# Performance work log

Hardware: AMD Instinct MI355X
Metric: run time of the kernel (lower is better)

Reference implementation:

```python
import jax, jax.numpy as jnp
from jax import lax
import numpy as np

# config (matches init_kwargs)
D_IN, D_OUT = 768, 128
P = 2
BLUR = 0.05
SCALING = 0.8
SCALING_FACTOR = 0.1
DIAM = 32.0  # static upper bound on transformed point-cloud diameter


def _eps_schedule():
    # geomloss-style epsilon annealing: eps from diameter**p down to blur**p
    eps_list = []
    eps = DIAM ** P
    target = BLUR ** P
    while eps > target:
        eps_list.append(eps)
        eps *= SCALING ** P
    eps_list.append(target)
    return np.asarray(eps_list, dtype=np.float32)


def _cost(x, y):
    # C_ij = (1/p) * ||x_i - y_j||^p with p=2 -> 0.5 * squared euclidean
    sq = (jnp.sum(x * x, -1)[:, None] + jnp.sum(y * y, -1)[None, :]
          - 2.0 * (x @ y.T))
    return 0.5 * jnp.maximum(sq, 0.0)


def _softmin(eps, C, h):
    # -eps * logsumexp_j( h_j - C_ij / eps ), rows of C
    return -eps * jax.nn.logsumexp(h[None, :] - C / eps, axis=1)


def sinkhorn_divergence(x, y):
    # Debiased Sinkhorn divergence S(x,y) = <a, f_xy - f_xx> + <b, g_xy - g_yy>
    # with uniform weights, log-domain iterations, eps-scaling, and
    # envelope-theorem gradients (loop runs on detached costs; one final
    # differentiable extrapolation) -- as in geomloss SamplesLoss('sinkhorn').
    eps_list = jnp.asarray(_eps_schedule())
    N, Mn = x.shape[0], y.shape[0]
    loga = jnp.float32(-np.log(N))
    logb = jnp.float32(-np.log(Mn))

    xd, yd = lax.stop_gradient(x), lax.stop_gradient(y)
    Cxy = _cost(xd, yd)   # [N, M]
    Cyx = Cxy.T           # [M, N]
    Cxx = _cost(xd, xd)   # [N, N]
    Cyy = _cost(yd, yd)   # [M, M]

    init = (jnp.zeros((N,), jnp.float32), jnp.zeros((Mn,), jnp.float32),
            jnp.zeros((N,), jnp.float32), jnp.zeros((Mn,), jnp.float32))

    def step(carry, eps):
        f, g, fx, gy = carry
        ft = _softmin(eps, Cxy, logb + g / eps)
        gt = _softmin(eps, Cyx, loga + f / eps)
        f2 = 0.5 * (f + ft)
        g2 = 0.5 * (g + gt)
        fx2 = 0.5 * (fx + _softmin(eps, Cxx, loga + fx / eps))
        gy2 = 0.5 * (gy + _softmin(eps, Cyy, logb + gy / eps))
        return (f2, g2, fx2, gy2), None

    (f, g, fx, gy), _ = lax.scan(step, init, eps_list)
    f, g, fx, gy = map(lax.stop_gradient, (f, g, fx, gy))

    eps = eps_list[-1]
    # final differentiable extrapolation through the cost
    f_xy = _softmin(eps, _cost(x, y), logb + g / eps)
    g_xy = _softmin(eps, _cost(y, x), loga + f / eps)
    f_xx = _softmin(eps, _cost(x, x), loga + fx / eps)
    g_yy = _softmin(eps, _cost(y, y), logb + gy / eps)
    return jnp.mean(f_xy - f_xx) + jnp.mean(g_xy - g_yy)


def setup_inputs() -> dict:
    key = jax.random.key(0)
    k1, k2, k3, k4 = jax.random.split(key, 4)
    d = jax.random.normal(k1, (4096, D_IN), jnp.float32)
    s1 = jax.random.normal(k2, (2048, D_IN), jnp.float32)
    s2 = jax.random.normal(k3, (2048, D_IN), jnp.float32)
    # learned metric transform M (scaled so transformed clouds have diam ~ DIAM)
    M = 0.02 * jax.random.normal(k4, (D_IN, D_OUT), jnp.float32)
    return {"d": d, "s1": s1, "s2": s2, "M": M}


def reference(d, s1, s2, M):
    td = d @ M
    t1 = s1 @ M
    t2 = s2 @ M
    dist1 = sinkhorn_divergence(td, t1)
    dist2 = sinkhorn_divergence(td, t2)
    return jax.nn.sigmoid(SCALING_FACTOR * (dist2 - dist1))
```

## Files before the change

kernel.cpp:

```cpp
#include <hip/hip_runtime.h>
#include <math.h>

typedef unsigned char u8;
typedef unsigned short u16;
typedef unsigned int u32;
typedef __attribute__((ext_vector_type(8))) short bf16x8;
typedef __attribute__((ext_vector_type(4))) float f32x4;

#define NE 30
static constexpr float QMAX  = 160.0f;
static constexpr float QS8   = 255.0f / QMAX;
static constexpr float HQS8  = 0.5f * QS8;
static constexpr float LOGA  = -8.3177661667193430f;
static constexpr float LOGB  = -7.6246189861593985f;
static constexpr float LOG2E = 1.4426950408889634f;
static constexpr float LN2   = 0.6931471805599453f;
static constexpr float LOGA2 = LOGA * LOG2E;
static constexpr float LOGB2 = LOGB * LOG2E;

static constexpr size_t OFF_MT  = 1048576;
static constexpr size_t OFF_N   = 1146880;
static constexpr size_t OFF_POT = 1155072;
static constexpr size_t OFF_OUT = 1187840;
static constexpr size_t OFF_CQ  = 1204224;
static constexpr size_t CQ_YX = 8388608;
static constexpr size_t CQ_YY = 16777216;
static constexpr size_t CQ_DV = 20971520;

__device__ __forceinline__ float fexp2(float x) {
#if __has_builtin(__builtin_amdgcn_exp2f)
  return __builtin_amdgcn_exp2f(x);
#else
  return exp2f(x);
#endif
}
__device__ __forceinline__ float flog2(float x) {
#if __has_builtin(__builtin_amdgcn_logf)
  return __builtin_amdgcn_logf(x);
#else
  return __log2f(x);
#endif
}

__device__ __forceinline__ void split1(float x, u16& h, u16& l) {
  const u32 u = __float_as_uint(x);
  const u32 hb = u & 0xffff0000u;
  const float xl = x - __uint_as_float(hb);
  h = (u16)(hb >> 16);
  l = (u16)(__float_as_uint(xl) >> 16);
}

__device__ __forceinline__ void splitAB(const float4 p, const float4 q,
                                        bf16x8& h, bf16x8& l) {
  const float pf[8] = {p.x, p.y, p.z, p.w, q.x, q.y, q.z, q.w};
#pragma unroll
  for (int i = 0; i < 8; ++i) {
    u16 hh, ll;
    split1(pf[i], hh, ll);
    h[i] = (short)hh;
    l[i] = (short)ll;
  }
}

__global__ __launch_bounds__(256) void prep_m_kernel(
    const float* __restrict__ Mw, float* __restrict__ ws)
{
  const int id = blockIdx.x * 256 + threadIdx.x;
  const int ks = id >> 9;
  const int g  = (id >> 7) & 3;
  const int n  = id & 127;
  u16* mthi = (u16*)(ws + OFF_MT);
  u16* mtlo = mthi + 98304;
  bf16x8 h, l;
#pragma unroll
  for (int e = 0; e < 8; ++e) {
    const float x = Mw[(size_t)(ks * 32 + g * 8 + e) * 128 + n];
    u16 hh, ll;
    split1(x, hh, ll);
    h[e] = (short)hh;
    l[e] = (short)ll;
  }
  *reinterpret_cast<bf16x8*>(mthi + (size_t)id * 8) = h;
  *reinterpret_cast<bf16x8*>(mtlo + (size_t)id * 8) = l;
}

__global__ __launch_bounds__(256) void transform_kernel(
    const float* __restrict__ d, const float* __restrict__ s1,
    const float* __restrict__ s2, float* __restrict__ ws)
{
  const int tid = threadIdx.x;
  const int w = tid >> 6, ln = tid & 63;
  const int lr = ln & 15, lg = ln >> 4;
  const int tile = blockIdx.x & 127;
  const int ks4  = blockIdx.x >> 7;
  const float* Xb; int r0;
  if (tile < 64)      { Xb = d;  r0 = tile * 64; }
  else if (tile < 96) { Xb = s1; r0 = (tile - 64) * 64; }
  else                { Xb = s2; r0 = (tile - 96) * 64; }
  const int grow = tile * 64;
  const u16* mthi = (const u16*)(ws + OFF_MT);
  const u16* mtlo = mthi + 98304;

  f32x4 acc[8];
  const f32x4 zero = {0.f, 0.f, 0.f, 0.f};
#pragma unroll
  for (int nt = 0; nt < 8; ++nt) acc[nt] = zero;

#pragma unroll
  for (int ksl = 0; ksl < 6; ++ksl) {
    const int ks = ks4 * 6 + ksl;
    const float* xp = Xb + (size_t)(r0 + w * 16 + lr) * 768 + ks * 32 + lg * 8;
    const float4 p = *reinterpret_cast<const float4*>(xp);
    const float4 q = *reinterpret_cast<const float4*>(xp + 4);
    bf16x8 ah, al;
    splitAB(p, q, ah, al);
#pragma unroll
    for (int nt = 0; nt < 8; ++nt) {
      const size_t bo = ((size_t)(ks * 4 + lg) * 128 + nt * 16 + lr) * 8;
      const bf16x8 bh = *reinterpret_cast<const bf16x8*>(mthi + bo);
      const bf16x8 bl = *reinterpret_cast<const bf16x8*>(mtlo + bo);
      acc[nt] = __builtin_amdgcn_mfma_f32_16x16x32_bf16(ah, bh, acc[nt], 0, 0, 0);
      acc[nt] = __builtin_amdgcn_mfma_f32_16x16x32_bf16(ah, bl, acc[nt], 0, 0, 0);
      acc[nt] = __builtin_amdgcn_mfma_f32_16x16x32_bf16(al, bh, acc[nt], 0, 0, 0);
    }
  }
  float* P = ws + OFF_CQ + (size_t)ks4 * 1048576;
#pragma unroll
  for (int nt = 0; nt < 8; ++nt)
#pragma unroll
    for (int reg = 0; reg < 4; ++reg)
      P[(size_t)(grow + w * 16 + lg * 4 + reg) * 128 + nt * 16 + lr] = acc[nt][reg];
}

__global__ __launch_bounds__(256) void reduceT_kernel(float* __restrict__ ws)
{
  const int wv = threadIdx.x >> 6, ln = threadIdx.x & 63;
  const int row = blockIdx.x * 4 + wv;
  const float2* Pb = reinterpret_cast<const float2*>(ws + OFF_CQ);
  const size_t idx = (size_t)row * 64 + ln;
  float2 t = Pb[idx];
  {
    const float2 b = Pb[idx + 524288];
    const float2 c = Pb[idx + 1048576];
    const float2 e = Pb[idx + 1572864];
    t.x += b.x + c.x + e.x;
    t.y += b.y + c.y + e.y;
  }
  float s = fmaf(t.x, t.x, t.y * t.y);
#pragma unroll
  for (int off = 32; off; off >>= 1) s += __shfl_xor(s, off);
  if (ln == 0) ws[OFF_N + row] = s;
  u16 h0, l0, h1, l1;
  split1(t.x, h0, l0);
  split1(t.y, h1, l1);
  u32* thiw = (u32*)ws;
  u32* tlow = thiw + 524288;
  thiw[idx] = (u32)h0 | ((u32)h1 << 16);
  tlow[idx] = (u32)l0 | ((u32)l1 << 16);
}

__global__ __launch_bounds__(256) void cost_all_kernel(float* __restrict__ ws)
{
  __shared__ __align__(16) float eb[16 * 516];
  const int tid = threadIdx.x;
  const int w = tid >> 6, ln = tid & 63;
  const int lr = ln & 15, lg = ln >> 4;

  const int b = blockIdx.x;
  const int dv = b / 1280;
  const int bb = b - dv * 1280;
  const u16* thi = (const u16*)ws;
  const u16* tlo = thi + 1048576;
  const u16* yhi = thi + (size_t)(4096 + dv * 2048) * 128;
  const u16* ylo = tlo + (size_t)(4096 + dv * 2048) * 128;
  const float* nrm = ws + OFF_N;
  u8* cq = (u8*)(ws + OFF_CQ) + (size_t)dv * CQ_DV;

  const u16 *xhi_, *xlo_, *yhi_, *ylo_;
  const float *nx, *ny;
  u8* C; int ldc, i0, j0;
  if (bb < 512) {
    i0 = (bb & 127) * 32; j0 = (bb >> 7) * 512;
    xhi_ = thi; xlo_ = tlo; yhi_ = yhi; ylo_ = ylo;
    nx = nrm; ny = nrm + 4096 + dv * 2048;
    C = cq; ldc = 2048;
  } else if (bb < 1024) {
    const int b2 = bb - 512;
    i0 = (b2 & 63) * 32; j0 = (b2 >> 6) * 512;
    xhi_ = yhi; xlo_ = ylo; yhi_ = thi; ylo_ = tlo;
    nx = nrm + 4096 + dv * 2048; ny = nrm;
    C = cq + CQ_YX; ldc = 4096;
  } else {
    const int b2 = bb - 1024;
    i0 = (b2 & 63) * 32; j0 = (b2 >> 6) * 512;
    xhi_ = yhi; xlo_ = ylo; yhi_ = yhi; ylo_ = ylo;
    nx = nrm + 4096 + dv * 2048; ny = nx;
    C = cq + CQ_YY; ldc = 2048;
  }
  const int cw = j0 + w * 128;

  f32x4 acc[2][8];
  const f32x4 zero = {0.f, 0.f, 0.f, 0.f};
#pragma unroll
  for (int mt = 0; mt < 2; ++mt)
#pragma unroll
    for (int nt = 0; nt < 8; ++nt) acc[mt][nt] = zero;

#pragma unroll
  for (int ks = 0; ks < 4; ++ks) {
    bf16x8 ah[2], al[2];
#pragma unroll
    for (int mt = 0; mt < 2; ++mt) {
      const size_t xo = (size_t)(i0 + mt * 16 + lr) * 128 + ks * 32 + lg * 8;
      ah[mt] = *reinterpret_cast<const bf16x8*>(xhi_ + xo);
      al[mt] = *reinterpret_cast<const bf16x8*>(xlo_ + xo);
    }
#pragma unroll
    for (int ntg = 0; ntg < 2; ++ntg) {
      bf16x8 bh[4], bl[4];
#pragma unroll
      for (int q = 0; q < 4; ++q) {
        const int nt = ntg * 4 + q;
        const size_t yo = (size_t)(cw + nt * 16 + lr) * 128 + ks * 32 + lg * 8;
        bh[q] = *reinterpret_cast<const bf16x8*>(yhi_ + yo);
        bl[q] = *reinterpret_cast<const bf16x8*>(ylo_ + yo);
      }
#pragma unroll
      for (int q = 0; q < 4; ++q) {
        const int nt = ntg * 4 + q;
#pragma unroll
        for (int mt = 0; mt < 2; ++mt) {
          acc[mt][nt] = __builtin_amdgcn_mfma_f32_16x16x32_bf16(ah[mt], bh[q], acc[mt][nt], 0, 0, 0);
          acc[mt][nt] = __builtin_amdgcn_mfma_f32_16x16x32_bf16(ah[mt], bl[q], acc[mt][nt], 0, 0, 0);
          acc[mt][nt] = __builtin_amdgcn_mfma_f32_16x16x32_bf16(al[mt], bh[q], acc[mt][nt], 0, 0, 0);
        }
      }
    }
  }

  float ct[8];
  {
    const float4 n0 = *reinterpret_cast<const float4*>(ny + j0 + ln * 8);
    const float4 n1 = *reinterpret_cast<const float4*>(ny + j0 + ln * 8 + 4);
    ct[0] = n0.x * HQS8; ct[1] = n0.y * HQS8; ct[2] = n0.z * HQS8; ct[3] = n0.w * HQS8;
    ct[4] = n1.x * HQS8; ct[5] = n1.y * HQS8; ct[6] = n1.z * HQS8; ct[7] = n1.w * HQS8;
  }

#pragma unroll
  for (int h = 0; h < 2; ++h) {
    if (h) __syncthreads();
#pragma unroll
    for (int nt = 0; nt < 8; ++nt)
#pragma unroll
      for (int reg = 0; reg < 4; ++reg)
        eb[(lg * 4 + reg) * 516 + w * 128 + nt * 16 + lr] = acc[h][nt][reg];
    __syncthreads();
#pragma unroll
    for (int rr = 0; rr < 4; ++rr) {
      const int rl = w * 4 + rr;
      const int rg = i0 + h * 16 + rl;
      const float rowt = fmaf(nx[rg], HQS8, 0.5f);
      const float* lp = eb + rl * 516 + ln * 8;
      const float4 e0 = *reinterpret_cast<const float4*>(lp);
      const float4 e1 = *reinterpret_cast<const float4*>(lp + 4);
      const float q0 = fmaxf(fminf(fmaf(e0.x, -QS8, ct[0] + rowt), 255.f), 0.f);
      const float q1 = fmaxf(fminf(fmaf(e0.y, -QS8, ct[1] + rowt), 255.f), 0.f);
      const float q2 = fmaxf(fminf(fmaf(e0.z, -QS8, ct[2] + rowt), 255.f), 0.f);
      const float q3 = fmaxf(fminf(fmaf(e0.w, -QS8, ct[3] + rowt), 255.f), 0.f);
      const float q4 = fmaxf(fminf(fmaf(e1.x, -QS8, ct[4] + rowt), 255.f), 0.f);
      const float q5 = fmaxf(fminf(fmaf(e1.y, -QS8, ct[5] + rowt), 255.f), 0.f);
      const float q6 = fmaxf(fminf(fmaf(e1.z, -QS8, ct[6] + rowt), 255.f), 0.f);
      const float q7 = fmaxf(fminf(fmaf(e1.w, -QS8, ct[7] + rowt), 255.f), 0.f);
      uint2 v;
      v.x = (u32)q0 | ((u32)q1 << 8) | ((u32)q2 << 16) | ((u32)q3 << 24);
      v.y = (u32)q4 | ((u32)q5 << 8) | ((u32)q6 << 16) | ((u32)q7 << 24);
      *reinterpret_cast<uint2*>(C + (size_t)rg * ldc + j0 + ln * 8) = v;
    }
  }
}

template <int NH>
__device__ __forceinline__ void softmin2(
    const u8* __restrict__ Cbase, const int ldc, const float* __restrict__ h,
    const float lw2, const float ie2, const float qie2, const float negeln2,
    const float* __restrict__ oldv, float* __restrict__ o,
    const int row0, const bool avg, const int ln)
{
  float m[2], s[2];
#pragma unroll
  for (int r = 0; r < 2; ++r) { m[r] = -3.0e38f; s[r] = 0.f; }
#pragma unroll
  for (int hf = 0; hf < NH; ++hf) {
    uint2 cq[2][4];
#pragma unroll
    for (int r = 0; r < 2; ++r) {
      const u8* cp = Cbase + (size_t)(row0 + r) * ldc + hf * 2048 + ln * 8;
#pragma unroll
      for (int k = 0; k < 4; ++k)
        cq[r][k] = *reinterpret_cast<const uint2*>(cp + k * 512);
    }
    const float* hp = h + hf * 2048 + ln * 8;
    float4 hv[8];
#pragma unroll
    for (int k = 0; k < 4; ++k) {
      hv[k * 2]     = *reinterpret_cast<const float4*>(hp + k * 512);
      hv[k * 2 + 1] = *reinterpret_cast<const float4*>(hp + k * 512 + 4);
    }
#pragma unroll
    for (int k = 0; k < 4; ++k) {
      float ht[8];
      ht[0] = fmaf(hv[k * 2].x, ie2, lw2);
      ht[1] = fmaf(hv[k * 2].y, ie2, lw2);
      ht[2] = fmaf(hv[k * 2].z, ie2, lw2);
      ht[3] = fmaf(hv[k * 2].w, ie2, lw2);
      ht[4] = fmaf(hv[k * 2 + 1].x, ie2, lw2);
      ht[5] = fmaf(hv[k * 2 + 1].y, ie2, lw2);
      ht[6] = fmaf(hv[k * 2 + 1].z, ie2, lw2);
      ht[7] = fmaf(hv[k * 2 + 1].w, ie2, lw2);
#pragma unroll
      for (int r = 0; r < 2; ++r) {
        const uint2 c = cq[r][k];
        const float a0 = ht[0] - (float)(c.x & 0xffu) * qie2;
        const float a1 = ht[1] - (float)((c.x >> 8) & 0xffu) * qie2;
        const float a2 = ht[2] - (float)((c.x >> 16) & 0xffu) * qie2;
        const float a3 = ht[3] - (float)(c.x >> 24) * qie2;
        const float a4 = ht[4] - (float)(c.y & 0xffu) * qie2;
        const float a5 = ht[5] - (float)((c.y >> 8) & 0xffu) * qie2;
        const float a6 = ht[6] - (float)((c.y >> 16) & 0xffu) * qie2;
        const float a7 = ht[7] - (float)(c.y >> 24) * qie2;
        const float cm = fmaxf(fmaxf(fmaxf(a0, a1), fmaxf(a2, a3)),
                               fmaxf(fmaxf(a4, a5), fmaxf(a6, a7)));
        const float nm = fmaxf(m[r], cm);
        float e = fexp2(a0 - nm);
        e += fexp2(a1 - nm);
        e += fexp2(a2 - nm);
        e += fexp2(a3 - nm);
        e += fexp2(a4 - nm);
        e += fexp2(a5 - nm);
        e += fexp2(a6 - nm);
        e += fexp2(a7 - nm);
        s[r] = fmaf(s[r], fexp2(m[r] - nm), e);
        m[r] = nm;
      }
    }
  }
#pragma unroll
  for (int r = 0; r < 2; ++r) {
#pragma unroll
    for (int off = 32; off; off >>= 1) {
      const float om = __shfl_xor(m[r], off);
      const float os = __shfl_xor(s[r], off);
      const float nm = fmaxf(m[r], om);
      s[r] = fmaf(s[r], fexp2(m[r] - nm), os * fexp2(om - nm));
      m[r] = nm;
    }
  }
  if (ln == 0) {
#pragma unroll
    for (int r = 0; r < 2; ++r) {
      float v = negeln2 * (m[r] + flog2(s[r]));
      if (avg) v = 0.5f * (oldv[row0 + r] + v);
      o[row0 + r] = v;
    }
  }
}

__global__ __launch_bounds__(256, 6) void sinkhorn_iter_kernel(
    float* __restrict__ ws, const float ie2, const float negeln2, const float qie2,
    const int cur, const int fin)
{
  const int w = threadIdx.x >> 6, ln = threadIdx.x & 63;
  const int dv = blockIdx.x >> 10;
  const int bb = blockIdx.x & 1023;
  float* pot  = ws + OFF_POT + dv * 16384;
  float* outv = ws + OFF_OUT + dv * 8192;
  const u8* cq = reinterpret_cast<const u8*>(ws + OFF_CQ) + (size_t)dv * CQ_DV;
  const float* fc = pot + cur * 4096;
  float* fn = pot + (cur ^ 1) * 4096;
  const float* gc = pot + 8192 + cur * 2048;
  float* gn = pot + 8192 + (cur ^ 1) * 2048;
  const float* yc = pot + 12288 + cur * 2048;
  float* yn = pot + 12288 + (cur ^ 1) * 2048;
  if (w == 0) {
    softmin2<2>(cq + CQ_YX, 4096, fc, LOGA2, ie2, qie2, negeln2,
                gc, fin ? (outv + 4096) : gn, bb * 2, !fin, ln);
  } else if (w == 3) {
    softmin2<1>(cq + CQ_YY, 2048, yc, LOGB2, ie2, qie2, negeln2,
                yc, fin ? (outv + 6144) : yn, bb * 2, !fin, ln);
  } else {
    softmin2<1>(cq, 2048, gc, LOGB2, ie2, qie2, negeln2,
                fc, fin ? outv : fn, bb * 4 + (w - 1) * 2, !fin, ln);
  }
}

__global__ void init_pot_kernel(float* __restrict__ ws)
{
  const int i = blockIdx.x * 256 + threadIdx.x;
  if (i < 32768) ws[OFF_POT + i] = 0.f;
}

__global__ __launch_bounds__(256) void finalize_kernel(
    const float* __restrict__ ws, float* __restrict__ out)
{
  const float* ov = ws + OFF_OUT;
  const int tid = threadIdx.x;
  float v[6] = {0.f, 0.f, 0.f, 0.f, 0.f, 0.f};
  for (int i = tid; i < 4096; i += 256) { v[0] += ov[i]; v[3] += ov[8192 + i]; }
  for (int i = tid; i < 2048; i += 256) {
    v[1] += ov[4096 + i]; v[2] += ov[6144 + i];
    v[4] += ov[8192 + 4096 + i]; v[5] += ov[8192 + 6144 + i];
  }
  __shared__ float sh[6][4];
  const int wv = tid >> 6, ln = tid & 63;
#pragma unroll
  for (int q = 0; q < 6; ++q) {
    float s = v[q];
#pragma unroll
    for (int off = 32; off; off >>= 1) s += __shfl_xor(s, off);
    if (ln == 0) sh[q][wv] = s;
  }
  __syncthreads();
  if (tid == 0) {
    float t[6];
#pragma unroll
    for (int q = 0; q < 6; ++q) t[q] = sh[q][0] + sh[q][1] + sh[q][2] + sh[q][3];
    const float d1 = t[0] * (1.f / 4096.f) + (t[1] - t[2]) * (1.f / 2048.f);
    const float d2 = t[3] * (1.f / 4096.f) + (t[4] - t[5]) * (1.f / 2048.f);
    const float z = 0.1f * (d2 - d1);
    out[0] = 1.f / (1.f + expf(-z));
  }
}

extern "C" void kernel_launch(void* const* d_in, const int* in_sizes, int n_in,
                              void* d_out, int out_size, void* d_ws, size_t ws_size,
                              hipStream_t stream)
{
  const float* d  = (const float*)d_in[0];
  const float* s1 = (const float*)d_in[1];
  const float* s2 = (const float*)d_in[2];
  const float* Mw = (const float*)d_in[3];
  float* out = (float*)d_out;
  float* ws = (float*)d_ws;

  float eps_l[NE];
  {
    double e = 1024.0;
    const double sc = 0.8 * 0.8;
    for (int k = 0; k < NE - 1; ++k) { eps_l[k] = (float)e; e *= sc; }
    eps_l[NE - 1] = (float)(0.05 * 0.05);
  }

  prep_m_kernel<<<48, 256, 0, stream>>>(Mw, ws);
  transform_kernel<<<512, 256, 0, stream>>>(d, s1, s2, ws);
  reduceT_kernel<<<2048, 256, 0, stream>>>(ws);

  cost_all_kernel<<<2560, 256, 0, stream>>>(ws);

  init_pot_kernel<<<128, 256, 0, stream>>>(ws);
  int cur = 0;
  for (int it = 0; it <= NE; ++it) {
    const int fin = (it == NE);
    const float e = eps_l[fin ? NE - 1 : it];
    const float ie2 = LOG2E / e;
    const float qie2 = (QMAX / 255.0f) * ie2;
    sinkhorn_iter_kernel<<<2048, 256, 0, stream>>>(ws, ie2, -e * LN2, qie2, cur, fin);
    if (!fin) cur ^= 1;
  }

  finalize_kernel<<<1, 256, 0, stream>>>(ws, out);
  (void)in_sizes; (void)n_in; (void)out_size; (void)ws_size;
}
```

Baseline: 512.3 us.

## Fuse Sinkhorn iterations into one persistent cooperative kernel with grid sync

Replaces the 31 per-iteration kernel launches with a single cooperative launch of 1280 blocks that loops over the epsilon schedule and uses grid-wide sync between iterations. The epsilon values now live in the workspace, written by the init kernel. Work is redistributed so each wave handles one uniform task (a full YX row, or two XY/YY rows) for both divergences, instead of a heterogeneous per-wave split. This removes launch overhead and inter-kernel gaps, at the cost of grid-barrier latency and an occupancy requirement of 5 blocks per CU, with a multi-launch fallback if the cooperative launch fails.

```diff
diff --git a/kernel.cpp b/kernel.cpp
--- a/kernel.cpp
+++ b/kernel.cpp
@@ -1,5 +1,8 @@
 #include <hip/hip_runtime.h>
+#include <hip/hip_cooperative_groups.h>
 #include <math.h>
+
+namespace cg = cooperative_groups;
 
 typedef unsigned char u8;
 typedef unsigned short u16;
@@ -19,6 +22,7 @@
 static constexpr float LOGB2 = LOGB * LOG2E;
 
 static constexpr size_t OFF_MT  = 1048576;
+static constexpr size_t OFF_EPS = 1048576;
 static constexpr size_t OFF_N   = 1146880;
 static constexpr size_t OFF_POT = 1155072;
 static constexpr size_t OFF_OUT = 1187840;
@@ -279,9 +283,69 @@
   }
 }
 
-template <int NH>
+__device__ __forceinline__ void softminR(
+    const u8* __restrict__ Crow, const float* __restrict__ h,
+    const float lw2, const float ie2, const float qie2, const float negeln2,
+    const float* __restrict__ oldv, float* __restrict__ o,
+    const int row, const bool avg, const int ln)
+{
+  float m = -3.0e38f, s = 0.f;
+#pragma unroll
+  for (int hf = 0; hf < 2; ++hf) {
+    const u8* cp = Crow + hf * 2048 + ln * 8;
+    const float* hp = h + hf * 2048 + ln * 8;
+    uint2 cq[4];
+#pragma unroll
+    for (int k = 0; k < 4; ++k)
+      cq[k] = *reinterpret_cast<const uint2*>(cp + k * 512);
+    float4 hv[8];
+#pragma unroll
+    for (int k = 0; k < 4; ++k) {
+      hv[k * 2]     = *reinterpret_cast<const float4*>(hp + k * 512);
+      hv[k * 2 + 1] = *reinterpret_cast<const float4*>(hp + k * 512 + 4);
+    }
+#pragma unroll
+    for (int k = 0; k < 4; ++k) {
+      const float a0 = fmaf(hv[k * 2].x, ie2, lw2) - (float)(cq[k].x & 0xffu) * qie2;
+      const float a1 = fmaf(hv[k * 2].y, ie2, lw2) - (float)((cq[k].x >> 8) & 0xffu) * qie2;
+      const float a2 = fmaf(hv[k * 2].z, ie2, lw2) - (float)((cq[k].x >> 16) & 0xffu) * qie2;
+      const float a3 = fmaf(hv[k * 2].w, ie2, lw2) - (float)(cq[k].x >> 24) * qie2;
+      const float a4 = fmaf(hv[k * 2 + 1].x, ie2, lw2) - (float)(cq[k].y & 0xffu) * qie2;
+      const float a5 = fmaf(hv[k * 2 + 1].y, ie2, lw2) - (float)((cq[k].y >> 8) & 0xffu) * qie2;
+      const float a6 = fmaf(hv[k * 2 + 1].z, ie2, lw2) - (float)((cq[k].y >> 16) & 0xffu) * qie2;
+      const float a7 = fmaf(hv[k * 2 + 1].w, ie2, lw2) - (float)(cq[k].y >> 24) * qie2;
+      const float cm = fmaxf(fmaxf(fmaxf(a0, a1), fmaxf(a2, a3)),
+                             fmaxf(fmaxf(a4, a5), fmaxf(a6, a7)));
+      const float nm = fmaxf(m, cm);
+      float e = fexp2(a0 - nm);
+      e += fexp2(a1 - nm);
+      e += fexp2(a2 - nm);
+      e += fexp2(a3 - nm);
+      e += fexp2(a4 - nm);
+      e += fexp2(a5 - nm);
+      e += fexp2(a6 - nm);
+      e += fexp2(a7 - nm);
+      s = fmaf(s, fexp2(m - nm), e);
+      m = nm;
+    }
+  }
+#pragma unroll
+  for (int off = 32; off; off >>= 1) {
+    const float om = __shfl_xor(m, off);
+    const float os = __shfl_xor(s, off);
+    const float nm = fmaxf(m, om);
+    s = fmaf(s, fexp2(m - nm), os * fexp2(om - nm));
+    m = nm;
+  }
+  if (ln == 0) {
+    float v = negeln2 * (m + flog2(s));
+    if (avg) v = 0.5f * (oldv[row] + v);
+    o[row] = v;
+  }
+}
+
 __device__ __forceinline__ void softmin2(
-    const u8* __restrict__ Cbase, const int ldc, const float* __restrict__ h,
+    const u8* __restrict__ Cbase, const float* __restrict__ h,
     const float lw2, const float ie2, const float qie2, const float negeln2,
     const float* __restrict__ oldv, float* __restrict__ o,
     const int row0, const bool avg, const int ln)
@@ -289,59 +353,56 @@
   float m[2], s[2];
 #pragma unroll
   for (int r = 0; r < 2; ++r) { m[r] = -3.0e38f; s[r] = 0.f; }
-#pragma unroll
-  for (int hf = 0; hf < NH; ++hf) {
-    uint2 cq[2][4];
+  uint2 cq[2][4];
+#pragma unroll
+  for (int r = 0; r < 2; ++r) {
+    const u8* cp = Cbase + (size_t)(row0 + r) * 2048 + ln * 8;
+#pragma unroll
+    for (int k = 0; k < 4; ++k)
+      cq[r][k] = *reinterpret_cast<const uint2*>(cp + k * 512);
+  }
+  const float* hp = h + ln * 8;
+  float4 hv[8];
+#pragma unroll
+  for (int k = 0; k < 4; ++k) {
+    hv[k * 2]     = *reinterpret_cast<const float4*>(hp + k * 512);
+    hv[k * 2 + 1] = *reinterpret_cast<const float4*>(hp + k * 512 + 4);
+  }
+#pragma unroll
+  for (int k = 0; k < 4; ++k) {
+    float ht[8];
+    ht[0] = fmaf(hv[k * 2].x, ie2, lw2);
+    ht[1] = fmaf(hv[k * 2].y, ie2, lw2);
+    ht[2] = fmaf(hv[k * 2].z, ie2, lw2);
+    ht[3] = fmaf(hv[k * 2].w, ie2, lw2);
+    ht[4] = fmaf(hv[k * 2 + 1].x, ie2, lw2);
+    ht[5] = fmaf(hv[k * 2 + 1].y, ie2, lw2);
+    ht[6] = fmaf(hv[k * 2 + 1].z, ie2, lw2);
+    ht[7] = fmaf(hv[k * 2 + 1].w, ie2, lw2);
 #pragma unroll
     for (int r = 0; r < 2; ++r) {
-      const u8* cp = Cbase + (size_t)(row0 + r) * ldc + hf * 2048 + ln * 8;
-#pragma unroll
-      for (int k = 0; k < 4; ++k)
-        cq[r][k] = *reinterpret_cast<const uint2*>(cp + k * 512);
-    }
-    const float* hp = h + hf * 2048 + ln * 8;
-    float4 hv[8];
-#pragma unroll
-    for (int k = 0; k < 4; ++k) {
-      hv[k * 2]     = *reinterpret_cast<const float4*>(hp + k * 512);
-      hv[k * 2 + 1] = *reinterpret_cast<const float4*>(hp + k * 512 + 4);
-    }
-#pragma unroll
-    for (int k = 0; k < 4; ++k) {
-      float ht[8];
-      ht[0] = fmaf(hv[k * 2].x, ie2, lw2);
-      ht[1] = fmaf(hv[k * 2].y, ie2, lw2);
-      ht[2] = fmaf(hv[k * 2].z, ie2, lw2);
-      ht[3] = fmaf(hv[k * 2].w, ie2, lw2);
-      ht[4] = fmaf(hv[k * 2 + 1].x, ie2, lw2);
-      ht[5] = fmaf(hv[k * 2 + 1].y, ie2, lw2);
-      ht[6] = fmaf(hv[k * 2 + 1].z, ie2, lw2);
-      ht[7] = fmaf(hv[k * 2 + 1].w, ie2, lw2);
-#pragma unroll
-      for (int r = 0; r < 2; ++r) {
-        const uint2 c = cq[r][k];
-        const float a0 = ht[0] - (float)(c.x & 0xffu) * qie2;
-        const float a1 = ht[1] - (float)((c.x >> 8) & 0xffu) * qie2;
-        const float a2 = ht[2] - (float)((c.x >> 16) & 0xffu) * qie2;
-        const float a3 = ht[3] - (float)(c.x >> 24) * qie2;
-        const float a4 = ht[4] - (float)(c.y & 0xffu) * qie2;
-        const float a5 = ht[5] - (float)((c.y >> 8) & 0xffu) * qie2;
-        const float a6 = ht[6] - (float)((c.y >> 16) & 0xffu) * qie2;
-        const float a7 = ht[7] - (float)(c.y >> 24) * qie2;
-        const float cm = fmaxf(fmaxf(fmaxf(a0, a1), fmaxf(a2, a3)),
-                               fmaxf(fmaxf(a4, a5), fmaxf(a6, a7)));
-        const float nm = fmaxf(m[r], cm);
-        float e = fexp2(a0 - nm);
-        e += fexp2(a1 - nm);
-        e += fexp2(a2 - nm);
-        e += fexp2(a3 - nm);
-        e += fexp2(a4 - nm);
-        e += fexp2(a5 - nm);
-        e += fexp2(a6 - nm);
-        e += fexp2(a7 - nm);
-        s[r] = fmaf(s[r], fexp2(m[r] - nm), e);
-        m[r] = nm;
-      }
+      const uint2 c = cq[r][k];
+      const float a0 = ht[0] - (float)(c.x & 0xffu) * qie2;
+      const float a1 = ht[1] - (float)((c.x >> 8) & 0xffu) * qie2;
+      const float a2 = ht[2] - (float)((c.x >> 16) & 0xffu) * qie2;
+      const float a3 = ht[3] - (float)(c.x >> 24) * qie2;
+      const float a4 = ht[4] - (float)(c.y & 0xffu) * qie2;
+      const float a5 = ht[5] - (float)((c.y >> 8) & 0xffu) * qie2;
+      const float a6 = ht[6] - (float)((c.y >> 16) & 0xffu) * qie2;
+      const float a7 = ht[7] - (float)(c.y >> 24) * qie2;
+      const float cm = fmaxf(fmaxf(fmaxf(a0, a1), fmaxf(a2, a3)),
+                             fmaxf(fmaxf(a4, a5), fmaxf(a6, a7)));
+      const float nm = fmaxf(m[r], cm);
+      float e = fexp2(a0 - nm);
+      e += fexp2(a1 - nm);
+      e += fexp2(a2 - nm);
+      e += fexp2(a3 - nm);
+      e += fexp2(a4 - nm);
+      e += fexp2(a5 - nm);
+      e += fexp2(a6 - nm);
+      e += fexp2(a7 - nm);
+      s[r] = fmaf(s[r], fexp2(m[r] - nm), e);
+      m[r] = nm;
     }
   }
 #pragma unroll
@@ -365,13 +426,11 @@
   }
 }
 
-__global__ __launch_bounds__(256, 6) void sinkhorn_iter_kernel(
-    float* __restrict__ ws, const float ie2, const float negeln2, const float qie2,
-    const int cur, const int fin)
-{
-  const int w = threadIdx.x >> 6, ln = threadIdx.x & 63;
-  const int dv = blockIdx.x >> 10;
-  const int bb = blockIdx.x & 1023;
+__device__ __forceinline__ void do_task(
+    float* __restrict__ ws, const int dv, const int tt,
+    const float ie2, const float negeln2, const float qie2,
+    const int cur, const int fin, const int ln)
+{
   float* pot  = ws + OFF_POT + dv * 16384;
   float* outv = ws + OFF_OUT + dv * 8192;
   const u8* cq = reinterpret_cast<const u8*>(ws + OFF_CQ) + (size_t)dv * CQ_DV;
@@ -381,15 +440,37 @@
   float* gn = pot + 8192 + (cur ^ 1) * 2048;
   const float* yc = pot + 12288 + cur * 2048;
   float* yn = pot + 12288 + (cur ^ 1) * 2048;
-  if (w == 0) {
-    softmin2<2>(cq + CQ_YX, 4096, fc, LOGA2, ie2, qie2, negeln2,
-                gc, fin ? (outv + 4096) : gn, bb * 2, !fin, ln);
-  } else if (w == 3) {
-    softmin2<1>(cq + CQ_YY, 2048, yc, LOGB2, ie2, qie2, negeln2,
-                yc, fin ? (outv + 6144) : yn, bb * 2, !fin, ln);
+  if (tt < 2048) {
+    softminR(cq + CQ_YX + (size_t)tt * 4096, fc, LOGA2, ie2, qie2, negeln2,
+             gc, fin ? (outv + 4096) : gn, tt, !fin, ln);
+  } else if (tt < 4096) {
+    softmin2(cq, gc, LOGB2, ie2, qie2, negeln2,
+             fc, fin ? outv : fn, (tt - 2048) * 2, !fin, ln);
   } else {
-    softmin2<1>(cq, 2048, gc, LOGB2, ie2, qie2, negeln2,
-                fc, fin ? outv : fn, bb * 4 + (w - 1) * 2, !fin, ln);
+    softmin2(cq + CQ_YY, yc, LOGB2, ie2, qie2, negeln2,
+             yc, fin ? (outv + 6144) : yn, (tt - 4096) * 2, !fin, ln);
+  }
+}
+
+__global__ __launch_bounds__(256, 5) void sink_coop_kernel(
+    float* __restrict__ ws, const int it0, const int it1)
+{
+  const int w = threadIdx.x >> 6, ln = threadIdx.x & 63;
+  const int gwid = blockIdx.x * 4 + w;
+  const float* eps = ws + OFF_EPS;
+  for (int it = it0; it <= it1; ++it) {
+    const int fin = (it == NE);
+    const float e = eps[fin ? NE - 1 : it];
+    const float ie2 = LOG2E / e;
+    const float qie2 = (QMAX / 255.0f) * ie2;
+    const float negeln2 = -e * LN2;
+    const int cur = it & 1;
+    do_task(ws, 0, gwid, ie2, negeln2, qie2, cur, fin, ln);
+    do_task(ws, 1, gwid, ie2, negeln2, qie2, cur, fin, ln);
+    if (it < it1) {
+      __threadfence();
+      cg::this_grid().sync();
+    }
   }
 }
 
@@ -397,6 +478,12 @@
 {
   const int i = blockIdx.x * 256 + threadIdx.x;
   if (i < 32768) ws[OFF_POT + i] = 0.f;
+  if (blockIdx.x == 0 && threadIdx.x == 0) {
+    double e = 1024.0;
+    const double sc = 0.8 * 0.8;
+    for (int k = 0; k < NE - 1; ++k) { ws[OFF_EPS + k] = (float)e; e *= sc; }
+    ws[OFF_EPS + NE - 1] = (float)(0.05 * 0.05);
+  }
 }
 
 __global__ __launch_bounds__(256) void finalize_kernel(
@@ -442,14 +529,6 @@
   float* out = (float*)d_out;
   float* ws = (float*)d_ws;
 
-  float eps_l[NE];
-  {
-    double e = 1024.0;
-    const double sc = 0.8 * 0.8;
-    for (int k = 0; k < NE - 1; ++k) { eps_l[k] = (float)e; e *= sc; }
-    eps_l[NE - 1] = (float)(0.05 * 0.05);
-  }
-
   prep_m_kernel<<<48, 256, 0, stream>>>(Mw, ws);
   transform_kernel<<<512, 256, 0, stream>>>(d, s1, s2, ws);
   reduceT_kernel<<<2048, 256, 0, stream>>>(ws);
@@ -457,14 +536,23 @@
   cost_all_kernel<<<2560, 256, 0, stream>>>(ws);
 
   init_pot_kernel<<<128, 256, 0, stream>>>(ws);
-  int cur = 0;
-  for (int it = 0; it <= NE; ++it) {
-    const int fin = (it == NE);
-    const float e = eps_l[fin ? NE - 1 : it];
-    const float ie2 = LOG2E / e;
-    const float qie2 = (QMAX / 255.0f) * ie2;
-    sinkhorn_iter_kernel<<<2048, 256, 0, stream>>>(ws, ie2, -e * LN2, qie2, cur, fin);
-    if (!fin) cur ^= 1;
+
+  bool coop_ok = false;
+  {
+    int maxB = 0;
+    hipError_t qe = hipOccupancyMaxActiveBlocksPerMultiprocessor(
+        &maxB, sink_coop_kernel, 256, 0);
+    if (qe == hipSuccess && maxB >= 5) {
+      int it0 = 0, it1 = NE;
+      void* args[] = { (void*)&ws, (void*)&it0, (void*)&it1 };
+      hipError_t le = hipLaunchCooperativeKernel(
+          (const void*)sink_coop_kernel, dim3(1280), dim3(256), args, 0, stream);
+      coop_ok = (le == hipSuccess);
+    }
+  }
+  if (!coop_ok) {
+    for (int it = 0; it <= NE; ++it)
+      sink_coop_kernel<<<1280, 256, 0, stream>>>(ws, it, it);
   }
 
   finalize_kernel<<<1, 256, 0, stream>>>(ws, out);
```

Result: slower. 573.8 us (+12.0%).

## Rebalance Sinkhorn softmin work per wave and widen loads to 16 bytes

Applied to the files above, without the earlier changes.

Before, each block gave its four waves fixed roles, and wave 0 handled the two 4096-wide YX rows while the other waves handled 2048-wide rows, so work per wave was uneven. Now each wave computes its task from a global wave id: one YX row per wave, or two rows of the 2048-wide XY/YY matrices, so every wave reads the same amount of data. The grid grows from 2048 to 2560 blocks. Cost loads widen from 8-byte uint2 to 16-byte uint4, with 16 columns per lane per chunk, which cuts the number of load instructions. In exchange, each lane now keeps 16 terms live in the log-sum-exp step, which may raise register pressure against the launch bound of 6.

```diff
diff --git a/kernel.cpp b/kernel.cpp
--- a/kernel.cpp
+++ b/kernel.cpp
@@ -279,70 +279,114 @@
   }
 }
 
-template <int NH>
+__device__ __forceinline__ void lse16c(
+    const uint4 c, const float* __restrict__ ht, const float qie2,
+    float& m, float& s)
+{
+  const float a0  = fmaf((float)(c.x & 0xffu),        -qie2, ht[0]);
+  const float a1  = fmaf((float)((c.x >> 8) & 0xffu), -qie2, ht[1]);
+  const float a2  = fmaf((float)((c.x >> 16) & 0xffu),-qie2, ht[2]);
+  const float a3  = fmaf((float)(c.x >> 24),          -qie2, ht[3]);
+  const float a4  = fmaf((float)(c.y & 0xffu),        -qie2, ht[4]);
+  const float a5  = fmaf((float)((c.y >> 8) & 0xffu), -qie2, ht[5]);
+  const float a6  = fmaf((float)((c.y >> 16) & 0xffu),-qie2, ht[6]);
+  const float a7  = fmaf((float)(c.y >> 24),          -qie2, ht[7]);
+  const float a8  = fmaf((float)(c.z & 0xffu),        -qie2, ht[8]);
+  const float a9  = fmaf((float)((c.z >> 8) & 0xffu), -qie2, ht[9]);
+  const float a10 = fmaf((float)((c.z >> 16) & 0xffu),-qie2, ht[10]);
+  const float a11 = fmaf((float)(c.z >> 24),          -qie2, ht[11]);
+  const float a12 = fmaf((float)(c.w & 0xffu),        -qie2, ht[12]);
+  const float a13 = fmaf((float)((c.w >> 8) & 0xffu), -qie2, ht[13]);
+  const float a14 = fmaf((float)((c.w >> 16) & 0xffu),-qie2, ht[14]);
+  const float a15 = fmaf((float)(c.w >> 24),          -qie2, ht[15]);
+  const float m0 = fmaxf(fmaxf(a0, a1), fmaxf(a2, a3));
+  const float m1 = fmaxf(fmaxf(a4, a5), fmaxf(a6, a7));
+  const float m2 = fmaxf(fmaxf(a8, a9), fmaxf(a10, a11));
+  const float m3 = fmaxf(fmaxf(a12, a13), fmaxf(a14, a15));
+  const float cm = fmaxf(fmaxf(m0, m1), fmaxf(m2, m3));
+  const float nm = fmaxf(m, cm);
+  float e = fexp2(a0 - nm);
+  e += fexp2(a1 - nm);  e += fexp2(a2 - nm);  e += fexp2(a3 - nm);
+  e += fexp2(a4 - nm);  e += fexp2(a5 - nm);  e += fexp2(a6 - nm);
+  e += fexp2(a7 - nm);  e += fexp2(a8 - nm);  e += fexp2(a9 - nm);
+  e += fexp2(a10 - nm); e += fexp2(a11 - nm); e += fexp2(a12 - nm);
+  e += fexp2(a13 - nm); e += fexp2(a14 - nm); e += fexp2(a15 - nm);
+  s = fmaf(s, fexp2(m - nm), e);
+  m = nm;
+}
+
+__device__ __forceinline__ void make_ht(
+    const float* __restrict__ hp, const float ie2, const float lw2,
+    float* __restrict__ ht)
+{
+  const float4 h0 = *reinterpret_cast<const float4*>(hp);
+  const float4 h1 = *reinterpret_cast<const float4*>(hp + 4);
+  const float4 h2 = *reinterpret_cast<const float4*>(hp + 8);
+  const float4 h3 = *reinterpret_cast<const float4*>(hp + 12);
+  ht[0]  = fmaf(h0.x, ie2, lw2); ht[1]  = fmaf(h0.y, ie2, lw2);
+  ht[2]  = fmaf(h0.z, ie2, lw2); ht[3]  = fmaf(h0.w, ie2, lw2);
+  ht[4]  = fmaf(h1.x, ie2, lw2); ht[5]  = fmaf(h1.y, ie2, lw2);
+  ht[6]  = fmaf(h1.z, ie2, lw2); ht[7]  = fmaf(h1.w, ie2, lw2);
+  ht[8]  = fmaf(h2.x, ie2, lw2); ht[9]  = fmaf(h2.y, ie2, lw2);
+  ht[10] = fmaf(h2.z, ie2, lw2); ht[11] = fmaf(h2.w, ie2, lw2);
+  ht[12] = fmaf(h3.x, ie2, lw2); ht[13] = fmaf(h3.y, ie2, lw2);
+  ht[14] = fmaf(h3.z, ie2, lw2); ht[15] = fmaf(h3.w, ie2, lw2);
+}
+
+__device__ __forceinline__ void softminR(
+    const u8* __restrict__ Crow, const float* __restrict__ h,
+    const float lw2, const float ie2, const float qie2, const float negeln2,
+    const float* __restrict__ oldv, float* __restrict__ o,
+    const int row, const bool avg, const int ln)
+{
+  const u8* cp = Crow + ln * 16;
+  uint4 cq[4];
+#pragma unroll
+  for (int k = 0; k < 4; ++k)
+    cq[k] = *reinterpret_cast<const uint4*>(cp + k * 1024);
+  float m = -3.0e38f, s = 0.f;
+#pragma unroll
+  for (int k = 0; k < 4; ++k) {
+    float ht[16];
+    make_ht(h + k * 1024 + ln * 16, ie2, lw2, ht);
+    lse16c(cq[k], ht, qie2, m, s);
+  }
+#pragma unroll
+  for (int off = 32; off; off >>= 1) {
+    const float om = __shfl_xor(m, off);
+    const float os = __shfl_xor(s, off);
+    const float nm = fmaxf(m, om);
+    s = fmaf(s, fexp2(m - nm), os * fexp2(om - nm));
+    m = nm;
+  }
+  if (ln == 0) {
+    float v = negeln2 * (m + flog2(s));
+    if (avg) v = 0.5f * (oldv[row] + v);
+    o[row] = v;
+  }
+}
+
 __device__ __forceinline__ void softmin2(
-    const u8* __restrict__ Cbase, const int ldc, const float* __restrict__ h,
+    const u8* __restrict__ Cbase, const float* __restrict__ h,
     const float lw2, const float ie2, const float qie2, const float negeln2,
     const float* __restrict__ oldv, float* __restrict__ o,
     const int row0, const bool avg, const int ln)
 {
-  float m[2], s[2];
-#pragma unroll
-  for (int r = 0; r < 2; ++r) { m[r] = -3.0e38f; s[r] = 0.f; }
-#pragma unroll
-  for (int hf = 0; hf < NH; ++hf) {
-    uint2 cq[2][4];
-#pragma unroll
-    for (int r = 0; r < 2; ++r) {
-      const u8* cp = Cbase + (size_t)(row0 + r) * ldc + hf * 2048 + ln * 8;
-#pragma unroll
-      for (int k = 0; k < 4; ++k)
-        cq[r][k] = *reinterpret_cast<const uint2*>(cp + k * 512);
-    }
-    const float* hp = h + hf * 2048 + ln * 8;
-    float4 hv[8];
-#pragma unroll
-    for (int k = 0; k < 4; ++k) {
-      hv[k * 2]     = *reinterpret_cast<const float4*>(hp + k * 512);
-      hv[k * 2 + 1] = *reinterpret_cast<const float4*>(hp + k * 512 + 4);
-    }
-#pragma unroll
-    for (int k = 0; k < 4; ++k) {
-      float ht[8];
-      ht[0] = fmaf(hv[k * 2].x, ie2, lw2);
-      ht[1] = fmaf(hv[k * 2].y, ie2, lw2);
-      ht[2] = fmaf(hv[k * 2].z, ie2, lw2);
-      ht[3] = fmaf(hv[k * 2].w, ie2, lw2);
-      ht[4] = fmaf(hv[k * 2 + 1].x, ie2, lw2);
-      ht[5] = fmaf(hv[k * 2 + 1].y, ie2, lw2);
-      ht[6] = fmaf(hv[k * 2 + 1].z, ie2, lw2);
-      ht[7] = fmaf(hv[k * 2 + 1].w, ie2, lw2);
-#pragma unroll
-      for (int r = 0; r < 2; ++r) {
-        const uint2 c = cq[r][k];
-        const float a0 = ht[0] - (float)(c.x & 0xffu) * qie2;
-        const float a1 = ht[1] - (float)((c.x >> 8) & 0xffu) * qie2;
-        const float a2 = ht[2] - (float)((c.x >> 16) & 0xffu) * qie2;
-        const float a3 = ht[3] - (float)(c.x >> 24) * qie2;
-        const float a4 = ht[4] - (float)(c.y & 0xffu) * qie2;
-        const float a5 = ht[5] - (float)((c.y >> 8) & 0xffu) * qie2;
-        const float a6 = ht[6] - (float)((c.y >> 16) & 0xffu) * qie2;
-        const float a7 = ht[7] - (float)(c.y >> 24) * qie2;
-        const float cm = fmaxf(fmaxf(fmaxf(a0, a1), fmaxf(a2, a3)),
-                               fmaxf(fmaxf(a4, a5), fmaxf(a6, a7)));
-        const float nm = fmaxf(m[r], cm);
-        float e = fexp2(a0 - nm);
-        e += fexp2(a1 - nm);
-        e += fexp2(a2 - nm);
-        e += fexp2(a3 - nm);
-        e += fexp2(a4 - nm);
-        e += fexp2(a5 - nm);
-        e += fexp2(a6 - nm);
-        e += fexp2(a7 - nm);
-        s[r] = fmaf(s[r], fexp2(m[r] - nm), e);
-        m[r] = nm;
-      }
-    }
+  uint4 cq[2][2];
+#pragma unroll
+  for (int r = 0; r < 2; ++r) {
+    const u8* cp = Cbase + (size_t)(row0 + r) * 2048 + ln * 16;
+#pragma unroll
+    for (int k = 0; k < 2; ++k)
+      cq[r][k] = *reinterpret_cast<const uint4*>(cp + k * 1024);
+  }
+  float m[2] = {-3.0e38f, -3.0e38f}, s[2] = {0.f, 0.f};
+#pragma unroll
+  for (int k = 0; k < 2; ++k) {
+    float ht[16];
+    make_ht(h + k * 1024 + ln * 16, ie2, lw2, ht);
+    lse16c(cq[0][k], ht, qie2, m[0], s[0]);
+    lse16c(cq[1][k], ht, qie2, m[1], s[1]);
   }
 #pragma unroll
   for (int r = 0; r < 2; ++r) {
@@ -370,8 +414,9 @@
     const int cur, const int fin)
 {
   const int w = threadIdx.x >> 6, ln = threadIdx.x & 63;
-  const int dv = blockIdx.x >> 10;
-  const int bb = blockIdx.x & 1023;
+  const int gwid = blockIdx.x * 4 + w;
+  const int dv = (gwid >= 5120) ? 1 : 0;
+  const int tt = gwid - dv * 5120;
   float* pot  = ws + OFF_POT + dv * 16384;
   float* outv = ws + OFF_OUT + dv * 8192;
   const u8* cq = reinterpret_cast<const u8*>(ws + OFF_CQ) + (size_t)dv * CQ_DV;
@@ -381,15 +426,15 @@
   float* gn = pot + 8192 + (cur ^ 1) * 2048;
   const float* yc = pot + 12288 + cur * 2048;
   float* yn = pot + 12288 + (cur ^ 1) * 2048;
-  if (w == 0) {
-    softmin2<2>(cq + CQ_YX, 4096, fc, LOGA2, ie2, qie2, negeln2,
-                gc, fin ? (outv + 4096) : gn, bb * 2, !fin, ln);
-  } else if (w == 3) {
-    softmin2<1>(cq + CQ_YY, 2048, yc, LOGB2, ie2, qie2, negeln2,
-                yc, fin ? (outv + 6144) : yn, bb * 2, !fin, ln);
+  if (tt < 2048) {
+    softminR(cq + CQ_YX + (size_t)tt * 4096, fc, LOGA2, ie2, qie2, negeln2,
+             gc, fin ? (outv + 4096) : gn, tt, !fin, ln);
+  } else if (tt < 4096) {
+    softmin2(cq, gc, LOGB2, ie2, qie2, negeln2,
+             fc, fin ? outv : fn, (tt - 2048) * 2, !fin, ln);
   } else {
-    softmin2<1>(cq, 2048, gc, LOGB2, ie2, qie2, negeln2,
-                fc, fin ? outv : fn, bb * 4 + (w - 1) * 2, !fin, ln);
+    softmin2(cq + CQ_YY, yc, LOGB2, ie2, qie2, negeln2,
+             yc, fin ? (outv + 6144) : yn, (tt - 4096) * 2, !fin, ln);
   }
 }
 
@@ -463,7 +508,7 @@
     const float e = eps_l[fin ? NE - 1 : it];
     const float ie2 = LOG2E / e;
     const float qie2 = (QMAX / 255.0f) * ie2;
-    sinkhorn_iter_kernel<<<2048, 256, 0, stream>>>(ws, ie2, -e * LN2, qie2, cur, fin);
+    sinkhorn_iter_kernel<<<2560, 256, 0, stream>>>(ws, ie2, -e * LN2, qie2, cur, fin);
     if (!fin) cur ^= 1;
   }
 
```

After: 522.8 us. 2.0% more time.
